# Kernel optimization log

Hardware: AMD Instinct MI355X
Metric: run time of the kernel (lower is better)

## Reference

```python
import jax, jax.numpy as jnp
import numpy as np

EMBED_DIM = 1024
NUM_HEADS = 16
HEAD_DIM = EMBED_DIM // NUM_HEADS


def setup_inputs() -> dict:
    key = jax.random.key(0)
    k1, k2, k3, k4, k5 = jax.random.split(key, 5)
    B, S, D = 2, 2048, EMBED_DIM
    s_in = 1.0 / np.sqrt(D)
    x = jax.random.normal(k1, (B, S, D), dtype=jnp.float32)
    W_qkv = jax.random.uniform(k2, (D, 3 * D), dtype=jnp.float32, minval=-s_in, maxval=s_in)
    b_qkv = jax.random.uniform(k3, (3 * D,), dtype=jnp.float32, minval=-s_in, maxval=s_in)
    W_out = jax.random.uniform(k4, (D, D), dtype=jnp.float32, minval=-s_in, maxval=s_in)
    b_out = jax.random.uniform(k5, (D,), dtype=jnp.float32, minval=-s_in, maxval=s_in)
    return {"x": x, "W_qkv": W_qkv, "b_qkv": b_qkv, "W_out": W_out, "b_out": b_out}


def reference(x, W_qkv, b_qkv, W_out, b_out):
    B, S, D = x.shape
    H, Hd = NUM_HEADS, HEAD_DIM
    qkv = x @ W_qkv + b_qkv                      # [B,S,3D]
    qkv = qkv.reshape(B, S, 3, H, Hd)
    q = qkv[:, :, 0].transpose(0, 2, 1, 3)       # [B,H,S,Hd]
    k = qkv[:, :, 1].transpose(0, 2, 1, 3)
    v = qkv[:, :, 2].transpose(0, 2, 1, 3)
    scores = jnp.einsum('bhsd,bhtd->bhst', q, k) / jnp.sqrt(jnp.float32(Hd))
    attn = jax.nn.softmax(scores, axis=-1)       # dropout is identity in eval mode
    out = jnp.einsum('bhst,bhtd->bhsd', attn, v)
    out = out.transpose(0, 2, 1, 3).reshape(B, S, D)
    return out @ W_out + b_out
```

## Files before the change

kernel.cpp:

```cpp
#include <hip/hip_runtime.h>
#include <stdint.h>
#include <math.h>

#define EMBED 1024
#define HEADS 16
#define HDIM  64
#define SEQ   2048
#define BATCH 2

typedef __bf16 bf16x8 __attribute__((ext_vector_type(8)));
typedef float  f32x4  __attribute__((ext_vector_type(4)));
typedef unsigned short u16x8 __attribute__((ext_vector_type(8)));
typedef unsigned short u16x4 __attribute__((ext_vector_type(4)));
typedef uint32_t u32x4v __attribute__((ext_vector_type(4)));

static __device__ __forceinline__ unsigned short f2bf(float f){
  union { float f; uint32_t u; } v; v.f = f;
  uint32_t u = v.u;
  uint32_t r = (u + 0x7FFFu + ((u >> 16) & 1u)) >> 16;
  return (unsigned short)r;
}
static __device__ __forceinline__ bf16x8 as_bf(u16x8 v){ return __builtin_bit_cast(bf16x8, v); }

static __device__ __forceinline__ uint32_t pk_bf16(float a, float b){
#if defined(__has_builtin) && __has_builtin(__builtin_amdgcn_cvt_pk_bf16_f32)
  typedef __bf16 bf16x2 __attribute__((ext_vector_type(2)));
  bf16x2 p = __builtin_amdgcn_cvt_pk_bf16_f32(a, b);
  return __builtin_bit_cast(uint32_t, p);
#else
  return (uint32_t)f2bf(a) | ((uint32_t)f2bf(b) << 16);
#endif
}

static __device__ __forceinline__ float fexp2(float x){
#if defined(__has_builtin) && __has_builtin(__builtin_amdgcn_exp2f)
  return __builtin_amdgcn_exp2f(x);
#else
  return exp2f(x);
#endif
}

static __device__ __forceinline__ void stage16(const unsigned short* gp,
                                               unsigned short* lp_wave, int lane){
#if defined(__has_builtin) && __has_builtin(__builtin_amdgcn_global_load_lds)
  __builtin_amdgcn_global_load_lds((const __attribute__((address_space(1))) void*)gp,
                                   (__attribute__((address_space(3))) void*)lp_wave,
                                   16, 0, 0);
#else
  *(u16x8*)(lp_wave + lane * 8) = *(const u16x8*)gp;
#endif
}

__global__ __launch_bounds__(256) void cast_x(const float* __restrict__ in,
                                              unsigned short* __restrict__ out){
  int i = (blockIdx.x * 256 + threadIdx.x) * 4;
  float4 v = *(const float4*)(in + i);
  u16x4 o;
  o[0] = f2bf(v.x); o[1] = f2bf(v.y); o[2] = f2bf(v.z); o[3] = f2bf(v.w);
  *(u16x4*)(out + i) = o;
}

__global__ __launch_bounds__(256) void wtrans(const float* __restrict__ W,
                                              unsigned short* __restrict__ Wt,
                                              int N, int K){
  __shared__ unsigned short T[32 * 36];
  int t = threadIdx.x;
  int n0 = blockIdx.x * 32, k0 = blockIdx.y * 32;
  int kr = t >> 3, nc = (t & 7) * 4;
  float4 wv = *(const float4*)(W + (size_t)(k0 + kr) * N + n0 + nc);
  T[(nc + 0) * 36 + kr] = f2bf(wv.x);
  T[(nc + 1) * 36 + kr] = f2bf(wv.y);
  T[(nc + 2) * 36 + kr] = f2bf(wv.z);
  T[(nc + 3) * 36 + kr] = f2bf(wv.w);
  __syncthreads();
  int nr = t >> 3, kc = (t & 7) * 4;
  *(u16x4*)(Wt + (size_t)(n0 + nr) * K + k0 + kc) = *(const u16x4*)&T[nr * 36 + kc];
}

__global__ __launch_bounds__(256) void vtrans(const unsigned short* __restrict__ V,
                                              unsigned short* __restrict__ VT){
  __shared__ unsigned short T[32 * 36];
  int t = threadIdx.x;
  int s0 = blockIdx.x * 32, d0 = blockIdx.y * 32;
  size_t base = (size_t)blockIdx.z * SEQ * HDIM;
  int sr = t >> 3, dc = (t & 7) * 4;
  u16x4 vv = *(const u16x4*)(V + base + (size_t)(s0 + sr) * HDIM + d0 + dc);
  T[(dc + 0) * 36 + sr] = vv[0];
  T[(dc + 1) * 36 + sr] = vv[1];
  T[(dc + 2) * 36 + sr] = vv[2];
  T[(dc + 3) * 36 + sr] = vv[3];
  __syncthreads();
  int dr = t >> 3, sc = (t & 7) * 4;
  int pos = (((sc >> 2) & 3) << 3) + (((sc >> 4) & 1) << 2);
  *(u16x4*)(VT + base + (size_t)(d0 + dr) * SEQ + s0 + pos) = *(const u16x4*)&T[dr * 36 + sc];
}

__global__ __launch_bounds__(256) void gemm_qkv(
    const unsigned short* __restrict__ A,
    const unsigned short* __restrict__ Bt,
    const float* __restrict__ bias,
    unsigned short* __restrict__ q_ws,
    unsigned short* __restrict__ k_ws,
    unsigned short* __restrict__ v_ws,
    int M, int N, int K)
{
  __shared__ unsigned short As[128 * 32];
  __shared__ unsigned short Bs[128 * 32];
  const int tid  = threadIdx.x;
  const int bm   = blockIdx.y, bn = blockIdx.x;
  const int w    = tid >> 6, lane = tid & 63;
  const int quad = lane >> 4, l16 = lane & 15;
  const int wm   = (w >> 1) * 64, wn = (w & 1) * 64;

  f32x4 acc[4][4] = {};

  for (int k0 = 0; k0 < K; k0 += 32) {
    #pragma unroll
    for (int i = 0; i < 2; i++){
      int c = w + i * 4;
      int row = c * 16 + (lane >> 2);
      int kg = (lane & 3) ^ (row & 3);
      stage16(A  + (size_t)(bm * 128 + row) * K + k0 + kg * 8, &As[c * 512], lane);
      stage16(Bt + (size_t)(bn * 128 + row) * K + k0 + kg * 8, &Bs[c * 512], lane);
    }
    __syncthreads();

    bf16x8 af[4], bfr[4];
    #pragma unroll
    for (int t = 0; t < 4; t++){
      int ra = wm + t * 16 + l16;
      int rb = wn + t * 16 + l16;
      af[t]  = as_bf(*(const u16x8*)&As[(ra << 5) + ((quad ^ (ra & 3)) << 3)]);
      bfr[t] = as_bf(*(const u16x8*)&Bs[(rb << 5) + ((quad ^ (rb & 3)) << 3)]);
    }
    #pragma unroll
    for (int mt = 0; mt < 4; mt++)
      #pragma unroll
      for (int nt = 0; nt < 4; nt++)
        acc[mt][nt] = __builtin_amdgcn_mfma_f32_16x16x32_bf16(af[mt], bfr[nt], acc[mt][nt], 0, 0, 0);
    __syncthreads();
  }

  const int which = (bn * 128) >> 10;
  unsigned short* dst = (which == 0) ? q_ws : (which == 1) ? k_ws : v_ws;
  const float scale = (which == 0) ? 0.18033688f : 1.0f;
  #pragma unroll
  for (int mt = 0; mt < 4; mt++){
    #pragma unroll
    for (int nt = 0; nt < 4; nt++){
      #pragma unroll
      for (int r = 0; r < 4; r++){
        int gm = bm * 128 + wm + mt * 16 + quad * 4 + r;
        int gn = bn * 128 + wn + nt * 16 + l16;
        int rem = gn & 1023;
        int h = rem >> 6, hd = rem & 63;
        int b = gm >> 11, s = gm & 2047;
        float val = (acc[mt][nt][r] + bias[gn]) * scale;
        dst[((size_t)(b * HEADS + h) * SEQ + s) * HDIM + hd] = f2bf(val);
      }
    }
  }
}

__global__ __launch_bounds__(256) void gemm_out(
    const unsigned short* __restrict__ A,
    const unsigned short* __restrict__ Bt,
    const float* __restrict__ bias,
    float* __restrict__ Cout,
    int M, int N, int K)
{
  __shared__ unsigned short As[128 * 32];
  __shared__ unsigned short Bs[64 * 32];
  const int tid  = threadIdx.x;
  const int bm   = blockIdx.y, bn = blockIdx.x;
  const int w    = tid >> 6, lane = tid & 63;
  const int quad = lane >> 4, l16 = lane & 15;
  const int wm   = (w >> 1) * 64, wn = (w & 1) * 32;

  f32x4 acc[4][2] = {};

  for (int k0 = 0; k0 < K; k0 += 32) {
    #pragma unroll
    for (int i = 0; i < 2; i++){
      int c = w + i * 4;
      int row = c * 16 + (lane >> 2);
      int kg = (lane & 3) ^ (row & 3);
      stage16(A + (size_t)(bm * 128 + row) * K + k0 + kg * 8, &As[c * 512], lane);
    }
    {
      int c = w;
      int row = c * 16 + (lane >> 2);
      int kg = (lane & 3) ^ (row & 3);
      stage16(Bt + (size_t)(bn * 64 + row) * K + k0 + kg * 8, &Bs[c * 512], lane);
    }
    __syncthreads();

    bf16x8 af[4], bfr[2];
    #pragma unroll
    for (int t = 0; t < 4; t++){
      int ra = wm + t * 16 + l16;
      af[t] = as_bf(*(const u16x8*)&As[(ra << 5) + ((quad ^ (ra & 3)) << 3)]);
    }
    #pragma unroll
    for (int t = 0; t < 2; t++){
      int rb = wn + t * 16 + l16;
      bfr[t] = as_bf(*(const u16x8*)&Bs[(rb << 5) + ((quad ^ (rb & 3)) << 3)]);
    }
    #pragma unroll
    for (int mt = 0; mt < 4; mt++)
      #pragma unroll
      for (int nt = 0; nt < 2; nt++)
        acc[mt][nt] = __builtin_amdgcn_mfma_f32_16x16x32_bf16(af[mt], bfr[nt], acc[mt][nt], 0, 0, 0);
    __syncthreads();
  }

  #pragma unroll
  for (int mt = 0; mt < 4; mt++)
    #pragma unroll
    for (int nt = 0; nt < 2; nt++)
      #pragma unroll
      for (int r = 0; r < 4; r++){
        int gm = bm * 128 + wm + mt * 16 + quad * 4 + r;
        int gn = bn * 64 + wn + nt * 16 + l16;
        Cout[(size_t)gm * N + gn] = acc[mt][nt][r] + bias[gn];
      }
}

__global__ __launch_bounds__(512) void attn(
    const unsigned short* __restrict__ q_ws,
    const unsigned short* __restrict__ k_ws,
    const unsigned short* __restrict__ vt_ws,
    unsigned short* __restrict__ o_ws)
{
  __shared__ unsigned short Qs[128 * 64];
  __shared__ unsigned short Ks[64 * 64];
  __shared__ unsigned short VTs[64 * 64];
  const int tid  = threadIdx.x;
  const int qt   = blockIdx.x, bh = blockIdx.y;
  const int w    = tid >> 6, lane = tid & 63;
  const int quad = lane >> 4, l16 = lane & 15;
  const size_t base = (size_t)bh * SEQ * HDIM;

  #pragma unroll
  for (int i = 0; i < 2; i++){
    int c = w * 2 + i;
    int row = c * 8 + (lane >> 3);
    int kg = (lane & 7) ^ (row & 7);
    stage16(q_ws + base + (size_t)(qt * 128 + row) * HDIM + kg * 8, &Qs[c * 512], lane);
  }

  const int srow = w * 8 + (lane >> 3);
  const int skg  = (lane & 7) ^ (srow & 7);

  stage16(k_ws  + base + (size_t)srow * HDIM + skg * 8, &Ks[w * 512],  lane);
  stage16(vt_ws + base + (size_t)srow * SEQ + skg * 8,  &VTs[w * 512], lane);
  __syncthreads();

  bf16x8 bq[2];
  {
    int row = w * 16 + l16;
    #pragma unroll
    for (int ks = 0; ks < 2; ks++)
      bq[ks] = as_bf(*(const u16x8*)&Qs[(row << 6) + ((((ks << 2) + quad) ^ (row & 7)) << 3)]);
  }

  f32x4 acc[4] = {};
  float li = 0.f;

  for (int kt = 0; kt < SEQ / 64; kt++){
    u16x8 kpre, vpre;
    if (kt < SEQ / 64 - 1){
      kpre = *(const u16x8*)(k_ws  + base + (size_t)((kt + 1) * 64 + srow) * HDIM + skg * 8);
      vpre = *(const u16x8*)(vt_ws + base + (size_t)srow * SEQ + (kt + 1) * 64 + skg * 8);
    }

    f32x4 sf[4] = {};
    #pragma unroll
    for (int ks = 0; ks < 2; ks++){
      #pragma unroll
      for (int nt = 0; nt < 4; nt++){
        int rk = nt * 16 + l16;
        bf16x8 ak = as_bf(*(const u16x8*)&Ks[(rk << 6) + ((((ks << 2) + quad) ^ (rk & 7)) << 3)]);
        sf[nt] = __builtin_amdgcn_mfma_f32_16x16x32_bf16(ak, bq[ks], sf[nt], 0, 0, 0);
      }
    }

    #pragma unroll
    for (int nt = 0; nt < 4; nt++)
      #pragma unroll
      for (int r = 0; r < 4; r++)
        sf[nt][r] = fexp2(sf[nt][r]);
    #pragma unroll
    for (int nt = 0; nt < 4; nt++)
      li += (sf[nt][0] + sf[nt][1]) + (sf[nt][2] + sf[nt][3]);

    #pragma unroll
    for (int c = 0; c < 2; c++){
      u32x4v aw;
      aw[0] = pk_bf16(sf[c * 2][0],     sf[c * 2][1]);
      aw[1] = pk_bf16(sf[c * 2][2],     sf[c * 2][3]);
      aw[2] = pk_bf16(sf[c * 2 + 1][0], sf[c * 2 + 1][1]);
      aw[3] = pk_bf16(sf[c * 2 + 1][2], sf[c * 2 + 1][3]);
      bf16x8 ap = __builtin_bit_cast(bf16x8, aw);
      #pragma unroll
      for (int nt = 0; nt < 4; nt++){
        int rv = nt * 16 + l16;
        bf16x8 bv = as_bf(*(const u16x8*)&VTs[(rv << 6) + ((((c << 2) + quad) ^ (rv & 7)) << 3)]);
        acc[nt] = __builtin_amdgcn_mfma_f32_16x16x32_bf16(ap, bv, acc[nt], 0, 0, 0);
      }
    }
    __syncthreads();

    if (kt < SEQ / 64 - 1){
      *(u16x8*)&Ks[w * 512 + lane * 8]  = kpre;
      *(u16x8*)&VTs[w * 512 + lane * 8] = vpre;
      __syncthreads();
    }
  }

  li += __shfl_xor(li, 16);
  li += __shfl_xor(li, 32);
  float inv = 1.0f / li;
  float invr[4];
  #pragma unroll
  for (int r = 0; r < 4; r++)
    invr[r] = __shfl(inv, quad * 4 + r);

  int b = bh >> 4, h = bh & 15;
  #pragma unroll
  for (int nt = 0; nt < 4; nt++)
    #pragma unroll
    for (int r = 0; r < 4; r++){
      int s = qt * 128 + w * 16 + quad * 4 + r;
      int d = h * 64 + nt * 16 + l16;
      o_ws[((size_t)(b * SEQ + s)) * EMBED + d] = f2bf(acc[nt][r] * invr[r]);
    }
}

extern "C" void kernel_launch(void* const* d_in, const int* in_sizes, int n_in,
                              void* d_out, int out_size, void* d_ws, size_t ws_size,
                              hipStream_t stream) {
  const float* x     = (const float*)d_in[0];
  const float* W_qkv = (const float*)d_in[1];
  const float* b_qkv = (const float*)d_in[2];
  const float* W_out = (const float*)d_in[3];
  const float* b_out = (const float*)d_in[4];
  float* out = (float*)d_out;

  char* ws = (char*)d_ws;
  unsigned short* xb    = (unsigned short*)(ws);
  unsigned short* q     = (unsigned short*)(ws + ((size_t)8  << 20));
  unsigned short* k     = (unsigned short*)(ws + ((size_t)16 << 20));
  unsigned short* v     = (unsigned short*)(ws + ((size_t)24 << 20));
  unsigned short* vt    = (unsigned short*)(ws + ((size_t)32 << 20));
  unsigned short* wqkvT = (unsigned short*)(ws + ((size_t)32 << 20));
  unsigned short* woutT = (unsigned short*)(ws + ((size_t)24 << 20));
  unsigned short* o     = xb;

  cast_x<<<dim3(4096), dim3(256), 0, stream>>>(x, xb);

  wtrans<<<dim3(96, 32), dim3(256), 0, stream>>>(W_qkv, wqkvT, 3072, 1024);

  gemm_qkv<<<dim3(24, 32), dim3(256), 0, stream>>>(
      xb, wqkvT, b_qkv, q, k, v, 4096, 3072, 1024);

  vtrans<<<dim3(64, 2, 32), dim3(256), 0, stream>>>(v, vt);

  wtrans<<<dim3(32, 32), dim3(256), 0, stream>>>(W_out, woutT, 1024, 1024);

  attn<<<dim3(16, 32), dim3(512), 0, stream>>>(q, k, vt, o);

  gemm_out<<<dim3(16, 32), dim3(256), 0, stream>>>(
      o, woutT, b_out, out, 4096, 1024, 1024);
}
```

Before: 202.4 us.

## Merge prep kernels, double-buffer attention K/V tiles, simplify QKV epilogue indexing

Merges the x cast and W_qkv transpose into one launch to cut a kernel launch. Double-buffers the K and V^T shared-memory tiles in the attention loop, so each iteration needs one barrier instead of two, and advances the prefetch pointers incrementally. Also hoists the bias load and head-index arithmetic out of the inner loops of the QKV GEMM epilogue. Double buffering doubles the K/V LDS footprint, which may lower occupancy.

```diff
diff --git a/kernel.cpp b/kernel.cpp
--- a/kernel.cpp
+++ b/kernel.cpp
@@ -51,30 +51,49 @@
 #endif
 }
 
-__global__ __launch_bounds__(256) void cast_x(const float* __restrict__ in,
-                                              unsigned short* __restrict__ out){
-  int i = (blockIdx.x * 256 + threadIdx.x) * 4;
-  float4 v = *(const float4*)(in + i);
-  u16x4 o;
-  o[0] = f2bf(v.x); o[1] = f2bf(v.y); o[2] = f2bf(v.z); o[3] = f2bf(v.w);
-  *(u16x4*)(out + i) = o;
-}
-
-__global__ __launch_bounds__(256) void wtrans(const float* __restrict__ W,
-                                              unsigned short* __restrict__ Wt,
-                                              int N, int K){
+__global__ __launch_bounds__(256) void prep(
+    const float* __restrict__ x,      unsigned short* __restrict__ xb,
+    const float* __restrict__ W_qkv,  unsigned short* __restrict__ wqkvT)
+{
   __shared__ unsigned short T[32 * 36];
-  int t = threadIdx.x;
-  int n0 = blockIdx.x * 32, k0 = blockIdx.y * 32;
+  const int bid = blockIdx.x;
+  const int t   = threadIdx.x;
+
+  if (bid < 4096){
+    int i = (bid * 256 + t) * 4;
+    float4 v = *(const float4*)(x + i);
+    u16x4 o;
+    o[0] = f2bf(v.x); o[1] = f2bf(v.y); o[2] = f2bf(v.z); o[3] = f2bf(v.w);
+    *(u16x4*)(xb + i) = o;
+    return;
+  }
+  int idx = bid - 4096;
+  int n0 = (idx % 96) * 32, k0 = (idx / 96) * 32;
   int kr = t >> 3, nc = (t & 7) * 4;
-  float4 wv = *(const float4*)(W + (size_t)(k0 + kr) * N + n0 + nc);
+  float4 wv = *(const float4*)(W_qkv + (size_t)(k0 + kr) * 3072 + n0 + nc);
   T[(nc + 0) * 36 + kr] = f2bf(wv.x);
   T[(nc + 1) * 36 + kr] = f2bf(wv.y);
   T[(nc + 2) * 36 + kr] = f2bf(wv.z);
   T[(nc + 3) * 36 + kr] = f2bf(wv.w);
   __syncthreads();
   int nr = t >> 3, kc = (t & 7) * 4;
-  *(u16x4*)(Wt + (size_t)(n0 + nr) * K + k0 + kc) = *(const u16x4*)&T[nr * 36 + kc];
+  *(u16x4*)(wqkvT + (size_t)(n0 + nr) * 1024 + k0 + kc) = *(const u16x4*)&T[nr * 36 + kc];
+}
+
+__global__ __launch_bounds__(256) void wtrans_out(const float* __restrict__ W,
+                                                  unsigned short* __restrict__ Wt){
+  __shared__ unsigned short T[32 * 36];
+  int t = threadIdx.x;
+  int n0 = blockIdx.x * 32, k0 = blockIdx.y * 32;
+  int kr = t >> 3, nc = (t & 7) * 4;
+  float4 wv = *(const float4*)(W + (size_t)(k0 + kr) * 1024 + n0 + nc);
+  T[(nc + 0) * 36 + kr] = f2bf(wv.x);
+  T[(nc + 1) * 36 + kr] = f2bf(wv.y);
+  T[(nc + 2) * 36 + kr] = f2bf(wv.z);
+  T[(nc + 3) * 36 + kr] = f2bf(wv.w);
+  __syncthreads();
+  int nr = t >> 3, kc = (t & 7) * 4;
+  *(u16x4*)(Wt + (size_t)(n0 + nr) * 1024 + k0 + kc) = *(const u16x4*)&T[nr * 36 + kc];
 }
 
 __global__ __launch_bounds__(256) void vtrans(const unsigned short* __restrict__ V,
@@ -144,20 +163,20 @@
   const int which = (bn * 128) >> 10;
   unsigned short* dst = (which == 0) ? q_ws : (which == 1) ? k_ws : v_ws;
   const float scale = (which == 0) ? 0.18033688f : 1.0f;
-  #pragma unroll
-  for (int mt = 0; mt < 4; mt++){
-    #pragma unroll
-    for (int nt = 0; nt < 4; nt++){
-      #pragma unroll
-      for (int r = 0; r < 4; r++){
-        int gm = bm * 128 + wm + mt * 16 + quad * 4 + r;
-        int gn = bn * 128 + wn + nt * 16 + l16;
-        int rem = gn & 1023;
-        int h = rem >> 6, hd = rem & 63;
-        int b = gm >> 11, s = gm & 2047;
-        float val = (acc[mt][nt][r] + bias[gn]) * scale;
-        dst[((size_t)(b * HEADS + h) * SEQ + s) * HDIM + hd] = f2bf(val);
-      }
+  const int b = bm >> 4;
+  #pragma unroll
+  for (int nt = 0; nt < 4; nt++){
+    int gnb = bn * 128 + wn + nt * 16;
+    int h   = (gnb & 1023) >> 6;
+    int hd  = (gnb & 63) + l16;
+    float bv = bias[gnb + l16];
+    unsigned short* dp = dst + (size_t)(b * HEADS + h) * SEQ * HDIM + hd;
+    #pragma unroll
+    for (int mt = 0; mt < 4; mt++){
+      int s0 = ((bm & 15) * 128) + wm + mt * 16 + quad * 4;
+      #pragma unroll
+      for (int r = 0; r < 4; r++)
+        dp[(size_t)(s0 + r) * HDIM] = f2bf((acc[mt][nt][r] + bv) * scale);
     }
   }
 }
@@ -233,8 +252,8 @@
     unsigned short* __restrict__ o_ws)
 {
   __shared__ unsigned short Qs[128 * 64];
-  __shared__ unsigned short Ks[64 * 64];
-  __shared__ unsigned short VTs[64 * 64];
+  __shared__ unsigned short Ks[2][64 * 64];
+  __shared__ unsigned short VTs[2][64 * 64];
   const int tid  = threadIdx.x;
   const int qt   = blockIdx.x, bh = blockIdx.y;
   const int w    = tid >> 6, lane = tid & 63;
@@ -251,9 +270,10 @@
 
   const int srow = w * 8 + (lane >> 3);
   const int skg  = (lane & 7) ^ (srow & 7);
-
-  stage16(k_ws  + base + (size_t)srow * HDIM + skg * 8, &Ks[w * 512],  lane);
-  stage16(vt_ws + base + (size_t)srow * SEQ + skg * 8,  &VTs[w * 512], lane);
+  const int dofs = w * 512 + lane * 8;
+
+  stage16(k_ws  + base + (size_t)srow * HDIM + skg * 8, &Ks[0][w * 512],  lane);
+  stage16(vt_ws + base + (size_t)srow * SEQ + skg * 8,  &VTs[0][w * 512], lane);
   __syncthreads();
 
   bf16x8 bq[2];
@@ -264,14 +284,18 @@
       bq[ks] = as_bf(*(const u16x8*)&Qs[(row << 6) + ((((ks << 2) + quad) ^ (row & 7)) << 3)]);
   }
 
+  const unsigned short* kp = k_ws  + base + (size_t)(64 + srow) * HDIM + skg * 8;
+  const unsigned short* vp = vt_ws + base + (size_t)srow * SEQ + 64 + skg * 8;
+
   f32x4 acc[4] = {};
   float li = 0.f;
 
   for (int kt = 0; kt < SEQ / 64; kt++){
+    const int cur = kt & 1;
     u16x8 kpre, vpre;
     if (kt < SEQ / 64 - 1){
-      kpre = *(const u16x8*)(k_ws  + base + (size_t)((kt + 1) * 64 + srow) * HDIM + skg * 8);
-      vpre = *(const u16x8*)(vt_ws + base + (size_t)srow * SEQ + (kt + 1) * 64 + skg * 8);
+      kpre = *(const u16x8*)kp;  kp += 64 * HDIM;
+      vpre = *(const u16x8*)vp;  vp += 64;
     }
 
     f32x4 sf[4] = {};
@@ -280,7 +304,7 @@
       #pragma unroll
       for (int nt = 0; nt < 4; nt++){
         int rk = nt * 16 + l16;
-        bf16x8 ak = as_bf(*(const u16x8*)&Ks[(rk << 6) + ((((ks << 2) + quad) ^ (rk & 7)) << 3)]);
+        bf16x8 ak = as_bf(*(const u16x8*)&Ks[cur][(rk << 6) + ((((ks << 2) + quad) ^ (rk & 7)) << 3)]);
         sf[nt] = __builtin_amdgcn_mfma_f32_16x16x32_bf16(ak, bq[ks], sf[nt], 0, 0, 0);
       }
     }
@@ -305,17 +329,16 @@
       #pragma unroll
       for (int nt = 0; nt < 4; nt++){
         int rv = nt * 16 + l16;
-        bf16x8 bv = as_bf(*(const u16x8*)&VTs[(rv << 6) + ((((c << 2) + quad) ^ (rv & 7)) << 3)]);
+        bf16x8 bv = as_bf(*(const u16x8*)&VTs[cur][(rv << 6) + ((((c << 2) + quad) ^ (rv & 7)) << 3)]);
         acc[nt] = __builtin_amdgcn_mfma_f32_16x16x32_bf16(ap, bv, acc[nt], 0, 0, 0);
       }
     }
-    __syncthreads();
 
     if (kt < SEQ / 64 - 1){
-      *(u16x8*)&Ks[w * 512 + lane * 8]  = kpre;
-      *(u16x8*)&VTs[w * 512 + lane * 8] = vpre;
-      __syncthreads();
-    }
+      *(u16x8*)&Ks[cur ^ 1][dofs]  = kpre;
+      *(u16x8*)&VTs[cur ^ 1][dofs] = vpre;
+    }
+    __syncthreads();
   }
 
   li += __shfl_xor(li, 16);
@@ -352,21 +375,19 @@
   unsigned short* q     = (unsigned short*)(ws + ((size_t)8  << 20));
   unsigned short* k     = (unsigned short*)(ws + ((size_t)16 << 20));
   unsigned short* v     = (unsigned short*)(ws + ((size_t)24 << 20));
+  unsigned short* woutT = (unsigned short*)(ws + ((size_t)24 << 20));
   unsigned short* vt    = (unsigned short*)(ws + ((size_t)32 << 20));
   unsigned short* wqkvT = (unsigned short*)(ws + ((size_t)32 << 20));
-  unsigned short* woutT = (unsigned short*)(ws + ((size_t)24 << 20));
   unsigned short* o     = xb;
 
-  cast_x<<<dim3(4096), dim3(256), 0, stream>>>(x, xb);
-
-  wtrans<<<dim3(96, 32), dim3(256), 0, stream>>>(W_qkv, wqkvT, 3072, 1024);
+  prep<<<dim3(7168), dim3(256), 0, stream>>>(x, xb, W_qkv, wqkvT);
 
   gemm_qkv<<<dim3(24, 32), dim3(256), 0, stream>>>(
       xb, wqkvT, b_qkv, q, k, v, 4096, 3072, 1024);
 
   vtrans<<<dim3(64, 2, 32), dim3(256), 0, stream>>>(v, vt);
 
-  wtrans<<<dim3(32, 32), dim3(256), 0, stream>>>(W_out, woutT, 1024, 1024);
+  wtrans_out<<<dim3(32, 32), dim3(256), 0, stream>>>(W_out, woutT);
 
   attn<<<dim3(16, 32), dim3(512), 0, stream>>>(q, k, vt, o);
 
```

Measured after the change: 198.0 us. 2.1% less time.
